# Kernel optimization log

Measured on AMD Instinct MI355X. Metric: run time of the kernel, lower is better.

The kernel has to match this reference:

```python
import jax, jax.numpy as jnp
import numpy as np

B, P, D = 128, 196, 2048      # batch, num_pixels (14*14), encoder_dim
A, E, H, V = 512, 512, 512, 10000  # attention_dim, embedding_size, lstm_size, vocab
T_MAX = 20
T = T_MAX - 1                 # decoder steps = max_length - 1


def setup_inputs() -> dict:
    key = jax.random.key(0)
    ks = jax.random.split(key, 24)
    s = lambda k, sh: (jax.random.normal(k, sh, jnp.float32) * 0.02)
    features = jax.random.normal(ks[0], (B, P, D), jnp.float32)
    captions = jax.random.randint(ks[1], (B, T_MAX), 0, V)
    # sorted-descending ragged lengths in [4, T_MAX]; force max to T_MAX
    lengths = jnp.sort(jax.random.randint(ks[2], (B,), 4, T_MAX + 1))[::-1].at[0].set(T_MAX)
    return dict(
        features=features, captions=captions, lengths=lengths,
        emb=s(ks[3], (V, E)),
        h_fc_w=s(ks[4], (D, H)), h_fc_b=jnp.zeros((H,), jnp.float32),
        c_fc_w=s(ks[5], (D, H)), c_fc_b=jnp.zeros((H,), jnp.float32),
        enc_w=s(ks[6], (D, A)), enc_b=jnp.zeros((A,), jnp.float32),
        dec_w=s(ks[7], (H, A)), dec_b=jnp.zeros((A,), jnp.float32),
        att_w=s(ks[8], (A, 1)), att_b=jnp.zeros((1,), jnp.float32),
        beta_w=s(ks[9], (H, D)), beta_b=jnp.zeros((D,), jnp.float32),
        w_ih=s(ks[10], (D + E, 4 * H)), b_ih=jnp.zeros((4 * H,), jnp.float32),
        w_hh=s(ks[11], (H, 4 * H)), b_hh=jnp.zeros((4 * H,), jnp.float32),
        cls_w=s(ks[12], (H, V)), cls_b=jnp.zeros((V,), jnp.float32),
    )


def reference(features, captions, lengths, emb,
              h_fc_w, h_fc_b, c_fc_w, c_fc_b,
              enc_w, enc_b, dec_w, dec_b, att_w, att_b,
              beta_w, beta_b, w_ih, b_ih, w_hh, b_hh, cls_w, cls_b):
    dec_len = lengths - 1                       # decoder_lengths
    mean_f = features.mean(axis=1)              # [B, D]
    h = mean_f @ h_fc_w + h_fc_b                # [B, H]
    c = mean_f @ c_fc_w + c_fc_b
    att1 = features @ enc_w + enc_b             # [B, P, A] (loop-invariant)
    emb_seq = emb[captions[:, :T]]              # [B, T, E]
    xs = (jnp.moveaxis(emb_seq, 0, 1),          # [T, B, E]
          jnp.arange(T)[:, None] < dec_len[None, :])  # [T, B] step-valid mask

    def step(carry, x):
        h, c = carry
        e_t, m = x                              # [B, E], [B] bool
        att2 = h @ dec_w + dec_b                # [B, A]
        e = jnp.squeeze(jax.nn.relu(att1 + att2[:, None, :]) @ att_w + att_b, -1)  # [B, P]
        alpha = jax.nn.softmax(e, axis=1)
        awe = jnp.einsum('bp,bpd->bd', alpha, features)
        gate = jax.nn.sigmoid(h @ beta_w + beta_b)
        awe = gate * awe
        xin = jnp.concatenate([e_t, awe], axis=1)           # [B, E+D]
        gates = xin @ w_ih + b_ih + h @ w_hh + b_hh         # [B, 4H]
        i, f, g, o = jnp.split(gates, 4, axis=1)
        c_new = jax.nn.sigmoid(f) * c + jax.nn.sigmoid(i) * jnp.tanh(g)
        h_new = jax.nn.sigmoid(o) * jnp.tanh(c_new)
        mf = m[:, None].astype(h.dtype)
        y = (h_new @ cls_w + cls_b) * mf        # rows past their length stay 0
        h = jnp.where(m[:, None], h_new, h)
        c = jnp.where(m[:, None], c_new, c)
        return (h, c), (y, alpha * mf)

    _, (ys, alphas) = jax.lax.scan(step, (h, c), xs)
    y_predicted = jnp.moveaxis(ys, 0, 1)        # [B, T, V]
    alphas = jnp.moveaxis(alphas, 0, 1)         # [B, T, P]
    return y_predicted, alphas
```

## Files before the change

kernel.cpp:

```cpp
#include <hip/hip_runtime.h>
#include <cstdint>
#include <cstddef>


#define DEV __device__ __forceinline__

typedef __attribute__((ext_vector_type(8))) short s16x8;
typedef __attribute__((ext_vector_type(4))) float f32x4;

constexpr int Bb = 128, Pp = 196, Dd = 2048, Aa = 512, Ee = 512, Hh = 512, Vv = 10000;
constexpr int Tt = 19, TMAX = 20;
constexpr int NVP = 10048;

DEV float fbs(short s) {
    union { uint32_t u; float f; } v;
    v.u = ((uint32_t)(uint16_t)s) << 16;
    return v.f;
}
DEV short bfs(float f) {
    union { float f; uint32_t u; } v;
    v.f = f;
    uint32_t u = v.u;
    uint32_t r = (u + 0x7FFFu + ((u >> 16) & 1u)) >> 16;
    return (short)(uint16_t)r;
}
DEV void upk(uint32_t v, float& lo, float& hi) {
    union { uint32_t u; float f; } a, b;
    a.u = v << 16;
    b.u = v & 0xffff0000u;
    lo = a.f;
    hi = b.f;
}

template<int BM, int BN, int BK, int TH, int WR, int WC, int EPI>
__global__ __launch_bounds__(TH) void gemm_k(
    const short* __restrict__ Ag, int lda,
    const short* __restrict__ Bg, int ldb,
    int K,
    float* __restrict__ outF, float* __restrict__ outF2,
    short* __restrict__ outH, short* __restrict__ outH2,
    int ldo,
    const float* __restrict__ bias, const float* __restrict__ bias2,
    const int* __restrict__ lens)
{
    constexpr int NCH = BK / 8;
    constexpr int AU = NCH * BM, BU = NCH * BN;
    constexpr int APT = AU / TH, BPT = BU / TH;
    constexpr int WM = BM / WR, WN = BN / WC;
    constexpr int FM = WM / 16, FN = WN / 16;

    __shared__ __align__(16) short sA[AU * 8];
    __shared__ __align__(16) short sB[BU * 8];

    const int tid = threadIdx.x, lane = tid & 63, wid = tid >> 6;
    const int l15 = lane & 15, l4 = lane >> 4;

    int m0, n0, trow_ = 0;
    if constexpr (EPI == 0) {
        int task = (blockIdx.x & 7) * 49 + (blockIdx.x >> 3);
        m0 = (task >> 1) * BM;
        n0 = (task & 1) * BN;
    } else if constexpr (EPI == 3) {
        const int nwg = (int)gridDim.x;
        const int qq = nwg >> 3, rr = nwg & 7;
        int xcd = (int)blockIdx.x & 7, idx = (int)blockIdx.x >> 3;
        int task = (xcd < rr) ? xcd * (qq + 1) + idx
                              : rr * (qq + 1) + (xcd - rr) * qq + idx;
        int npanel = task / Tt;
        trow_ = task - npanel * Tt;
        m0 = trow_ * BM;
        n0 = npanel * BN;
    } else if constexpr (EPI == 4) {
        m0 = ((int)blockIdx.x & 3) * BM;
        n0 = ((int)blockIdx.x >> 2) * BN;
    } else {
        m0 = blockIdx.y * BM;
        n0 = blockIdx.x * BN;
    }
    const int wr = wid / WC, wc = wid % WC;

    f32x4 acc[FM][FN];
    #pragma unroll
    for (int i = 0; i < FM; ++i)
        #pragma unroll
        for (int j = 0; j < FN; ++j) acc[i][j] = {0.f, 0.f, 0.f, 0.f};

    for (int kt = 0; kt < K; kt += BK) {
        s16x8 ra[APT], rb[BPT];
        #pragma unroll
        for (int i = 0; i < APT; ++i) {
            int q2 = tid + TH * i;
            int r2 = q2 / NCH, ch = q2 % NCH;
            ra[i] = *(const s16x8*)(Ag + (size_t)(m0 + r2) * lda + kt + ch * 8);
        }
        #pragma unroll
        for (int i = 0; i < BPT; ++i) {
            int q2 = tid + TH * i;
            int r2 = q2 / NCH, ch = q2 % NCH;
            rb[i] = *(const s16x8*)(Bg + (size_t)(n0 + r2) * ldb + kt + ch * 8);
        }
        __syncthreads();
        #pragma unroll
        for (int i = 0; i < APT; ++i) {
            int q2 = tid + TH * i;
            int r2 = q2 / NCH, ch = q2 % NCH;
            *(s16x8*)(sA + (r2 * NCH + (ch ^ (r2 & 7))) * 8) = ra[i];
        }
        #pragma unroll
        for (int i = 0; i < BPT; ++i) {
            int q2 = tid + TH * i;
            int r2 = q2 / NCH, ch = q2 % NCH;
            *(s16x8*)(sB + (r2 * NCH + (ch ^ (r2 & 7))) * 8) = rb[i];
        }
        __syncthreads();
        #pragma unroll
        for (int ks = 0; ks < BK / 32; ++ks) {
            s16x8 af[FM], bf[FN];
            #pragma unroll
            for (int fm = 0; fm < FM; ++fm) {
                int rr2 = wr * WM + fm * 16 + l15, cc = ks * 4 + l4;
                af[fm] = *(const s16x8*)&sA[(rr2 * NCH + (cc ^ (rr2 & 7))) * 8];
            }
            #pragma unroll
            for (int fn = 0; fn < FN; ++fn) {
                int rr2 = wc * WN + fn * 16 + l15, cc = ks * 4 + l4;
                bf[fn] = *(const s16x8*)&sB[(rr2 * NCH + (cc ^ (rr2 & 7))) * 8];
            }
            #pragma unroll
            for (int fm = 0; fm < FM; ++fm)
                #pragma unroll
                for (int fn = 0; fn < FN; ++fn)
                    acc[fm][fn] = __builtin_amdgcn_mfma_f32_16x16x32_bf16(af[fm], bf[fn], acc[fm][fn], 0, 0, 0);
        }
        __syncthreads();
    }

    #pragma unroll
    for (int fm = 0; fm < FM; ++fm)
        #pragma unroll
        for (int fn = 0; fn < FN; ++fn)
            #pragma unroll
            for (int r2 = 0; r2 < 4; ++r2) {
                int ml = wr * WM + fm * 16 + l4 * 4 + r2;
                int nl = wc * WN + fn * 16 + l15;
                int m = m0 + ml, n = n0 + nl;
                float v = acc[fm][fn][r2];
                if constexpr (EPI == 0) {
                    outH[(size_t)m * ldo + n] = bfs(v + bias[n]);
                } else if constexpr (EPI == 1) {
                    outH[(size_t)m * ldo + n] = bfs(v);
                } else if constexpr (EPI == 3) {
                    if (n < Vv) {
                        bool mk = trow_ < lens[ml] - 1;
                        outF[((size_t)ml * Tt + trow_) * Vv + n] = mk ? (v + bias[n]) : 0.f;
                    }
                } else if constexpr (EPI == 4) {
                    if (n < 512) outF[(size_t)m * Aa + n] = v + bias[n];
                    else if (n < 2560)
                        outF2[(size_t)m * Dd + (n - 512)] =
                            1.f / (1.f + expf(-(v + bias2[n - 512])));
                    else
                        ((float*)outH)[(size_t)m * 2048 + (n - 2560)] = v;
                } else if constexpr (EPI == 6) {
                    if (n < 512) {
                        outH2[(size_t)m * 512 + n] = bfs(v + bias[n]);
                    } else {
                        outF2[(size_t)m * 512 + (n - 512)] = v + bias2[n - 512];
                    }
                }
            }
}

__global__ __launch_bounds__(512) void att_awe_k(
    const short* __restrict__ att1b, const float* __restrict__ att2b,
    const float* __restrict__ att_w, const float* __restrict__ att_b,
    const short* __restrict__ featb, const float* __restrict__ gatebuf,
    short* __restrict__ xin, float* __restrict__ al_out,
    const int* __restrict__ lens, int t)
{
    const int b = blockIdx.y, half = blockIdx.x;
    const int tid = threadIdx.x, lane = tid & 63, wid = tid >> 6;
    __shared__ float se[224];
    __shared__ float sred[256];
    __shared__ float sal[224];

    float aw[8], a2[8];
    #pragma unroll
    for (int j = 0; j < 8; ++j) {
        aw[j] = att_w[lane * 8 + j];
        a2[j] = att2b[b * 512 + lane * 8 + j];
    }
    float ab = att_b[0];
    for (int p = wid; p < Pp; p += 8) {
        s16x8 row = *(const s16x8*)&att1b[((size_t)b * Pp + p) * 512 + lane * 8];
        float s = 0.f;
        #pragma unroll
        for (int j = 0; j < 8; ++j) {
            float v = fbs(row[j]) + a2[j];
            v = v > 0.f ? v : 0.f;
            s += v * aw[j];
        }
        #pragma unroll
        for (int m = 32; m; m >>= 1) s += __shfl_xor(s, m);
        if (lane == 0) se[p] = s + ab;
    }
    __syncthreads();
    float e = 0.f, ex = 0.f;
    if (tid < 256) {
        e = (tid < Pp) ? se[tid] : -3.0e38f;
        sred[tid] = e;
    }
    __syncthreads();
    for (int st = 128; st > 0; st >>= 1) {
        if (tid < st) sred[tid] = fmaxf(sred[tid], sred[tid + st]);
        __syncthreads();
    }
    float mx = sred[0];
    __syncthreads();
    if (tid < 256) {
        ex = (tid < Pp) ? expf(e - mx) : 0.f;
        sred[tid] = ex;
    }
    __syncthreads();
    for (int st = 128; st > 0; st >>= 1) {
        if (tid < st) sred[tid] += sred[tid + st];
        __syncthreads();
    }
    float inv = 1.f / sred[0];
    if (tid < Pp) {
        float al = ex * inv;
        sal[tid] = al;
        if (half == 0) {
            float mf = (t < lens[b] - 1) ? 1.f : 0.f;
            al_out[((size_t)b * Tt + t) * Pp + tid] = al * mf;
        }
    }
    __syncthreads();
    int d0 = half * 1024 + tid * 2;
    const short* f = featb + (size_t)b * Pp * Dd + d0;
    float s0 = 0.f, s1 = 0.f;
    #pragma unroll 4
    for (int p = 0; p < Pp; ++p) {
        uint32_t v = *(const uint32_t*)(f + (size_t)p * Dd);
        float lo, hi;
        upk(v, lo, hi);
        float al = sal[p];
        s0 += al * lo;
        s1 += al * hi;
    }
    float2 g = *(const float2*)&gatebuf[b * 2048 + d0];
    uint32_t o = ((uint32_t)(uint16_t)bfs(g.y * s1) << 16) | (uint16_t)bfs(g.x * s0);
    *(uint32_t*)(xin + (size_t)b * 2048 + d0) = o;
}

__global__ __launch_bounds__(256) void gates_lstm_k(
    const short* __restrict__ xin, const short* __restrict__ combT,
    const short* __restrict__ eprec, const float* __restrict__ hpart,
    const float* __restrict__ b_ih, const float* __restrict__ b_hh,
    float* __restrict__ c_state, short* __restrict__ hnew_all,
    short* __restrict__ hb16, const int* __restrict__ lens, int t)
{
    constexpr int BM = 32, BN = 32, BK = 128, K = 2048;
    constexpr int NCH = BK / 8;
    constexpr int AU = NCH * BM;
    __shared__ __align__(16) short sA[AU * 8];
    __shared__ __align__(16) short sB[AU * 8];

    const int m0 = ((int)blockIdx.x & 3) * BM, n0 = ((int)blockIdx.x >> 2) * BN;
    const int tid = threadIdx.x, lane = tid & 63, wid = tid >> 6;
    const int l15 = lane & 15, l4 = lane >> 4;
    const int wr = wid >> 1, wc = wid & 1;

    f32x4 acc = {0.f, 0.f, 0.f, 0.f};
    const int r2 = tid / NCH, ch0 = tid % NCH;
    const short* Abase = xin + (size_t)(m0 + r2) * 2048 + ch0 * 8;
    const short* Bbase = combT + (size_t)(n0 + r2) * 2048 + ch0 * 8;
    const size_t rowadv = (size_t)16 * 2048;

    s16x8 raA0, raA1, rbA0, rbA1, raB0, raB1, rbB0, rbB1;

    auto loadA = [&](int kt, s16x8& a0, s16x8& a1, s16x8& b0, s16x8& b1) {
        a0 = *(const s16x8*)(Abase + kt);
        a1 = *(const s16x8*)(Abase + rowadv + kt);
        b0 = *(const s16x8*)(Bbase + kt);
        b1 = *(const s16x8*)(Bbase + rowadv + kt);
    };
    const int sl0 = ((r2) * NCH + (ch0 ^ (r2 & 7))) * 8;
    const int sl1 = ((r2 + 16) * NCH + (ch0 ^ ((r2 + 16) & 7))) * 8;
    auto storeS = [&](s16x8& a0, s16x8& a1, s16x8& b0, s16x8& b1) {
        *(s16x8*)(sA + sl0) = a0;
        *(s16x8*)(sA + sl1) = a1;
        *(s16x8*)(sB + sl0) = b0;
        *(s16x8*)(sB + sl1) = b1;
    };
    const int rrA = wr * 16 + l15, rrB = wc * 16 + l15;
    auto mfmaS = [&]() {
        #pragma unroll
        for (int ks = 0; ks < BK / 32; ++ks) {
            int cc = ks * 4 + l4;
            s16x8 af = *(const s16x8*)&sA[(rrA * NCH + (cc ^ (rrA & 7))) * 8];
            s16x8 bf = *(const s16x8*)&sB[(rrB * NCH + (cc ^ (rrB & 7))) * 8];
            acc = __builtin_amdgcn_mfma_f32_16x16x32_bf16(af, bf, acc, 0, 0, 0);
        }
    };

    loadA(0, raA0, raA1, rbA0, rbA1);
    #pragma unroll 1
    for (int kt = 0; kt < K; kt += 2 * BK) {
        __syncthreads();
        storeS(raA0, raA1, rbA0, rbA1);
        __syncthreads();
        if (kt + BK < K) loadA(kt + BK, raB0, raB1, rbB0, rbB1);
        mfmaS();
        __syncthreads();
        storeS(raB0, raB1, rbB0, rbB1);
        __syncthreads();
        if (kt + 2 * BK < K) loadA(kt + 2 * BK, raA0, raA1, rbA0, rbA1);
        mfmaS();
    }

    __syncthreads();
    float* sE = (float*)sA;
    #pragma unroll
    for (int r = 0; r < 4; ++r) {
        int ml = wr * 16 + l4 * 4 + r, nl = wc * 16 + l15;
        sE[ml * 32 + nl] = acc[r];
    }
    __syncthreads();
    int bl = tid >> 3, jl = tid & 7;
    int b = m0 + bl, q = (n0 >> 2) + jl;
    f32x4 ge = *(const f32x4*)&sE[bl * 32 + jl * 4];
    f32x4 hp = *(const f32x4*)&hpart[(size_t)b * 2048 + n0 + jl * 4];
    short4 ep = *(const short4*)&eprec[((size_t)t * 128 + b) * 2048 + n0 + jl * 4];
    float gi = ge[0] + hp[0] + fbs(ep.x) + b_ih[q]        + b_hh[q];
    float gf = ge[1] + hp[1] + fbs(ep.y) + b_ih[512 + q]  + b_hh[512 + q];
    float gg = ge[2] + hp[2] + fbs(ep.z) + b_ih[1024 + q] + b_hh[1024 + q];
    float go = ge[3] + hp[3] + fbs(ep.w) + b_ih[1536 + q] + b_hh[1536 + q];
    float si = 1.f / (1.f + expf(-gi));
    float sf = 1.f / (1.f + expf(-gf));
    float so = 1.f / (1.f + expf(-go));
    float tg = tanhf(gg);
    int sidx = b * 512 + q;
    float cn = sf * c_state[sidx] + si * tg;
    float hn = so * tanhf(cn);
    hnew_all[((size_t)t * 128 + b) * 512 + q] = bfs(hn);
    if (t < lens[b] - 1) {
        c_state[sidx] = cn;
        hb16[sidx] = bfs(hn);
    }
}

__global__ __launch_bounds__(256) void conv_mean_k(
    const float* __restrict__ feat, short* __restrict__ featb, short* __restrict__ meanb)
{
    int b = blockIdx.y;
    int d = (blockIdx.x * 256 + threadIdx.x) * 2;
    const float* f = feat + (size_t)b * Pp * Dd + d;
    short* o = featb + (size_t)b * Pp * Dd + d;
    float s0 = 0.f, s1 = 0.f;
    #pragma unroll 4
    for (int p = 0; p < Pp; ++p) {
        float2 v = *(const float2*)(f + (size_t)p * Dd);
        s0 += v.x; s1 += v.y;
        uint32_t ov = ((uint32_t)(uint16_t)bfs(v.y) << 16) | (uint16_t)bfs(v.x);
        *(uint32_t*)(o + (size_t)p * Dd) = ov;
    }
    const float inv = 1.f / 196.f;
    uint32_t mv = ((uint32_t)(uint16_t)bfs(s1 * inv) << 16) | (uint16_t)bfs(s0 * inv);
    *(uint32_t*)(meanb + (size_t)b * Dd + d) = mv;
}

DEV void t32(const float* __restrict__ src, int R, int C,
             short* __restrict__ dst, int ds, int off, int perm,
             int local, int gx, float (*tile)[33])
{
    int x = local % gx, y = local / gx;
    int c0 = x * 32, r0 = y * 32;
    int tx = threadIdx.x & 31, ty = threadIdx.x >> 5;
    #pragma unroll
    for (int i = 0; i < 4; ++i) {
        int r = r0 + ty + i * 8, c = c0 + tx;
        tile[ty + i * 8][tx] = (r < R && c < C) ? src[(size_t)r * C + c] : 0.f;
    }
    __syncthreads();
    #pragma unroll
    for (int i = 0; i < 4; ++i) {
        int cc = c0 + ty + i * 8, rr = r0 + tx;
        if (rr < R) {
            int drow = perm ? ((cc & 511) * 4 + (cc >> 9)) : cc;
            dst[(size_t)drow * ds + off + rr] = bfs(tile[tx][ty + i * 8]);
        }
    }
}

__global__ __launch_bounds__(256) void prep_k(
    const float* __restrict__ enc_w, const float* __restrict__ h_fc_w,
    const float* __restrict__ c_fc_w, const float* __restrict__ dec_w,
    const float* __restrict__ beta_w, const float* __restrict__ w_ih,
    const float* __restrict__ w_hh, const float* __restrict__ cls_w,
    const float* __restrict__ emb, const int* __restrict__ caps,
    short* __restrict__ encT, short* __restrict__ hcT, short* __restrict__ catT,
    short* __restrict__ combT, short* __restrict__ wtopT, short* __restrict__ clsT,
    short* __restrict__ embseq)
{
    __shared__ float tile[32][33];
    int bid = blockIdx.x;
    if (bid < 1024)        t32(enc_w, 2048, 512, encT, 2048, 0, 0, bid, 16, tile);
    else if (bid < 2048)   t32(h_fc_w, 2048, 512, hcT, 2048, 0, 0, bid - 1024, 16, tile);
    else if (bid < 3072)   t32(c_fc_w, 2048, 512, hcT + (size_t)512 * 2048, 2048, 0, 0, bid - 2048, 16, tile);
    else if (bid < 3328)   t32(dec_w, 512, 512, catT, 512, 0, 0, bid - 3072, 16, tile);
    else if (bid < 4352)   t32(beta_w, 512, 2048, catT + (size_t)512 * 512, 512, 0, 0, bid - 3328, 64, tile);
    else if (bid < 5376)   t32(w_hh, 512, 2048, catT + (size_t)2560 * 512, 512, 0, 1, bid - 4352, 64, tile);
    else if (bid < 9472)   t32(w_ih + (size_t)512 * 2048, 2048, 2048, combT, 2048, 0, 1, bid - 5376, 64, tile);
    else if (bid < 10496)  t32(w_ih, 512, 2048, wtopT, 512, 0, 1, bid - 9472, 64, tile);
    else if (bid < 15520)  t32(cls_w, 512, 10000, clsT, 512, 0, 0, bid - 10496, 314, tile);
    else {
        size_t i = (size_t)(bid - 15520) * 256 + threadIdx.x;
        if (i < (size_t)Tt * Bb * Ee) {
            int e = (int)(i % Ee);
            size_t r = i / Ee;
            int b = (int)(r % Bb);
            int t = (int)(r / Bb);
            int cap = caps[b * TMAX + t];
            embseq[i] = bfs(emb[(size_t)cap * Ee + e]);
        }
    }
}

extern "C" void kernel_launch(void* const* d_in, const int* in_sizes, int n_in,
                              void* d_out, int out_size, void* d_ws, size_t ws_size,
                              hipStream_t stream)
{
    const float* features = (const float*)d_in[0];
    const int* captions   = (const int*)d_in[1];
    const int* lengths    = (const int*)d_in[2];
    const float* emb      = (const float*)d_in[3];
    const float* h_fc_w   = (const float*)d_in[4];
    const float* h_fc_b   = (const float*)d_in[5];
    const float* c_fc_w   = (const float*)d_in[6];
    const float* c_fc_b   = (const float*)d_in[7];
    const float* enc_w    = (const float*)d_in[8];
    const float* enc_b    = (const float*)d_in[9];
    const float* dec_w    = (const float*)d_in[10];
    const float* dec_b    = (const float*)d_in[11];
    const float* att_w    = (const float*)d_in[12];
    const float* att_b    = (const float*)d_in[13];
    const float* beta_w   = (const float*)d_in[14];
    const float* beta_b   = (const float*)d_in[15];
    const float* w_ih     = (const float*)d_in[16];
    const float* b_ih     = (const float*)d_in[17];
    const float* w_hh     = (const float*)d_in[18];
    const float* b_hh     = (const float*)d_in[19];
    const float* cls_w    = (const float*)d_in[20];
    const float* cls_b    = (const float*)d_in[21];

    char* w = (char*)d_ws;
    auto alloc = [&](size_t bytes) {
        char* p = w;
        w += (bytes + 255) & ~(size_t)255;
        return p;
    };
    short* featb    = (short*)alloc((size_t)Bb * Pp * Dd * 2);
    short* att1b    = (short*)alloc((size_t)Bb * Pp * Aa * 2);
    short* encT     = (short*)alloc((size_t)Aa * Dd * 2);
    short* combT    = (short*)alloc((size_t)2048 * 2048 * 2);
    short* wtopT    = (short*)alloc((size_t)2048 * 512 * 2);
    short* clsT     = (short*)alloc((size_t)NVP * Hh * 2);
    short* catT     = (short*)alloc((size_t)4608 * 512 * 2);
    short* hcT      = (short*)alloc((size_t)1024 * Dd * 2);
    short* embseq   = (short*)alloc((size_t)Tt * Bb * Ee * 2);
    short* meanb    = (short*)alloc((size_t)Bb * Dd * 2);
    short* eprec    = (short*)alloc((size_t)Tt * Bb * 2048 * 2);
    float* c_state  = (float*)alloc((size_t)Bb * Hh * 4);
    float* att2b    = (float*)alloc((size_t)Bb * Aa * 4);
    float* gatebuf  = (float*)alloc((size_t)Bb * Dd * 4);
    float* hpart    = (float*)alloc((size_t)Bb * 2048 * 4);
    short* xin      = (short*)alloc((size_t)Bb * 2048 * 2);
    short* hb16     = (short*)alloc((size_t)Bb * Hh * 2);
    short* hnew_all = (short*)alloc((size_t)Tt * Bb * Hh * 2);

    float* y_out  = (float*)d_out;
    float* al_out = y_out + (size_t)Bb * Tt * Vv;

    conv_mean_k<<<dim3(4, 128), 256, 0, stream>>>(features, featb, meanb);
    prep_k<<<dim3(20384), 256, 0, stream>>>(
        enc_w, h_fc_w, c_fc_w, dec_w, beta_w, w_ih, w_hh, cls_w, emb, captions,
        encT, hcT, catT, combT, wtopT, clsT, embseq);

    gemm_k<128, 64, 64, 256, 2, 2, 6><<<dim3(16, 1), 256, 0, stream>>>(
        meanb, 2048, hcT, 2048, 2048,
        nullptr, c_state, nullptr, hb16, 0, h_fc_b, c_fc_b, nullptr);

    gemm_k<128, 256, 64, 512, 2, 4, 0><<<dim3(392), 512, 0, stream>>>(
        featb, 2048, encT, 2048, 2048,
        nullptr, nullptr, att1b, nullptr, Aa, enc_b, nullptr, nullptr);

    gemm_k<128, 64, 64, 256, 2, 2, 1><<<dim3(32, 19), 256, 0, stream>>>(
        embseq, 512, wtopT, 512, 512,
        nullptr, nullptr, eprec, nullptr, 2048, nullptr, nullptr, nullptr);

    for (int t = 0; t < Tt; ++t) {
        gemm_k<32, 64, 64, 256, 2, 2, 4><<<dim3(288), 256, 0, stream>>>(
            hb16, 512, catT, 512, 512,
            att2b, gatebuf, (short*)hpart, nullptr, 0, dec_b, beta_b, nullptr);
        att_awe_k<<<dim3(2, 128), 512, 0, stream>>>(
            att1b, att2b, att_w, att_b, featb, gatebuf, xin,
            al_out, lengths, t);
        gates_lstm_k<<<dim3(256), 256, 0, stream>>>(
            xin, combT, eprec, hpart, b_ih, b_hh, c_state, hnew_all, hb16,
            lengths, t);
    }

    gemm_k<128, 64, 64, 256, 2, 2, 3><<<dim3(157 * Tt), 256, 0, stream>>>(
        hnew_all, 512, clsT, 512, 512,
        y_out, nullptr, nullptr, nullptr, 0, cls_b, nullptr, lengths);
}
```

Before: 1.356 ms.

## Prefetch GEMM tiles into registers, merge attention halves, widen classifier tiles

The GEMM main loop now issues the global loads for the next K tile into a second register set while MFMAs run on the current shared-memory tile, hiding global latency. The attention/AWE kernel uses one 1024-thread block per batch row instead of two 512-thread blocks, so the energy and softmax phase is no longer computed twice. The classifier GEMM moves to 128-wide N tiles, with vocab padding raised to 10112 and the prep transpose grid adjusted to match. Risks include higher register pressure from the doubled prefetch buffers, and the two-tiles-per-iteration loop assumes K is a multiple of 2*BK.

Result: faster. 1.239 ms (-8.6%).

```diff
diff --git a/kernel.cpp b/kernel.cpp
--- a/kernel.cpp
+++ b/kernel.cpp
@@ -10,7 +10,7 @@
 
 constexpr int Bb = 128, Pp = 196, Dd = 2048, Aa = 512, Ee = 512, Hh = 512, Vv = 10000;
 constexpr int Tt = 19, TMAX = 20;
-constexpr int NVP = 10048;
+constexpr int NVP = 10112;
 
 DEV float fbs(short s) {
     union { uint32_t u; float f; } v;
@@ -85,34 +85,37 @@
         #pragma unroll
         for (int j = 0; j < FN; ++j) acc[i][j] = {0.f, 0.f, 0.f, 0.f};
 
-    for (int kt = 0; kt < K; kt += BK) {
-        s16x8 ra[APT], rb[BPT];
+    s16x8 ra[APT], rb[BPT], ra2[APT], rb2[BPT];
+
+    auto gload = [&](int kt, s16x8 (&pa)[APT], s16x8 (&pb)[BPT]) {
         #pragma unroll
         for (int i = 0; i < APT; ++i) {
             int q2 = tid + TH * i;
             int r2 = q2 / NCH, ch = q2 % NCH;
-            ra[i] = *(const s16x8*)(Ag + (size_t)(m0 + r2) * lda + kt + ch * 8);
+            pa[i] = *(const s16x8*)(Ag + (size_t)(m0 + r2) * lda + kt + ch * 8);
         }
         #pragma unroll
         for (int i = 0; i < BPT; ++i) {
             int q2 = tid + TH * i;
             int r2 = q2 / NCH, ch = q2 % NCH;
-            rb[i] = *(const s16x8*)(Bg + (size_t)(n0 + r2) * ldb + kt + ch * 8);
-        }
-        __syncthreads();
+            pb[i] = *(const s16x8*)(Bg + (size_t)(n0 + r2) * ldb + kt + ch * 8);
+        }
+    };
+    auto sstore = [&](s16x8 (&pa)[APT], s16x8 (&pb)[BPT]) {
         #pragma unroll
         for (int i = 0; i < APT; ++i) {
             int q2 = tid + TH * i;
             int r2 = q2 / NCH, ch = q2 % NCH;
-            *(s16x8*)(sA + (r2 * NCH + (ch ^ (r2 & 7))) * 8) = ra[i];
+            *(s16x8*)(sA + (r2 * NCH + (ch ^ (r2 & 7))) * 8) = pa[i];
         }
         #pragma unroll
         for (int i = 0; i < BPT; ++i) {
             int q2 = tid + TH * i;
             int r2 = q2 / NCH, ch = q2 % NCH;
-            *(s16x8*)(sB + (r2 * NCH + (ch ^ (r2 & 7))) * 8) = rb[i];
-        }
-        __syncthreads();
+            *(s16x8*)(sB + (r2 * NCH + (ch ^ (r2 & 7))) * 8) = pb[i];
+        }
+    };
+    auto domfma = [&]() {
         #pragma unroll
         for (int ks = 0; ks < BK / 32; ++ks) {
             s16x8 af[FM], bf[FN];
@@ -132,7 +135,21 @@
                 for (int fn = 0; fn < FN; ++fn)
                     acc[fm][fn] = __builtin_amdgcn_mfma_f32_16x16x32_bf16(af[fm], bf[fn], acc[fm][fn], 0, 0, 0);
         }
-        __syncthreads();
+    };
+
+    gload(0, ra, rb);
+    #pragma unroll 1
+    for (int kt = 0; kt < K; kt += 2 * BK) {
+        __syncthreads();
+        sstore(ra, rb);
+        __syncthreads();
+        gload(kt + BK, ra2, rb2);
+        domfma();
+        __syncthreads();
+        sstore(ra2, rb2);
+        __syncthreads();
+        if (kt + 2 * BK < K) gload(kt + 2 * BK, ra, rb);
+        domfma();
     }
 
     #pragma unroll
@@ -171,14 +188,14 @@
             }
 }
 
-__global__ __launch_bounds__(512) void att_awe_k(
+__global__ __launch_bounds__(1024) void att_awe_k(
     const short* __restrict__ att1b, const float* __restrict__ att2b,
     const float* __restrict__ att_w, const float* __restrict__ att_b,
     const short* __restrict__ featb, const float* __restrict__ gatebuf,
     short* __restrict__ xin, float* __restrict__ al_out,
     const int* __restrict__ lens, int t)
 {
-    const int b = blockIdx.y, half = blockIdx.x;
+    const int b = blockIdx.x;
     const int tid = threadIdx.x, lane = tid & 63, wid = tid >> 6;
     __shared__ float se[224];
     __shared__ float sred[256];
@@ -191,7 +208,7 @@
         a2[j] = att2b[b * 512 + lane * 8 + j];
     }
     float ab = att_b[0];
-    for (int p = wid; p < Pp; p += 8) {
+    for (int p = wid; p < Pp; p += 16) {
         s16x8 row = *(const s16x8*)&att1b[((size_t)b * Pp + p) * 512 + lane * 8];
         float s = 0.f;
         #pragma unroll
@@ -230,13 +247,11 @@
     if (tid < Pp) {
         float al = ex * inv;
         sal[tid] = al;
-        if (half == 0) {
-            float mf = (t < lens[b] - 1) ? 1.f : 0.f;
-            al_out[((size_t)b * Tt + t) * Pp + tid] = al * mf;
-        }
-    }
-    __syncthreads();
-    int d0 = half * 1024 + tid * 2;
+        float mf = (t < lens[b] - 1) ? 1.f : 0.f;
+        al_out[((size_t)b * Tt + t) * Pp + tid] = al * mf;
+    }
+    __syncthreads();
+    int d0 = tid * 2;
     const short* f = featb + (size_t)b * Pp * Dd + d0;
     float s0 = 0.f, s1 = 0.f;
     #pragma unroll 4
@@ -413,9 +428,9 @@
     else if (bid < 5376)   t32(w_hh, 512, 2048, catT + (size_t)2560 * 512, 512, 0, 1, bid - 4352, 64, tile);
     else if (bid < 9472)   t32(w_ih + (size_t)512 * 2048, 2048, 2048, combT, 2048, 0, 1, bid - 5376, 64, tile);
     else if (bid < 10496)  t32(w_ih, 512, 2048, wtopT, 512, 0, 1, bid - 9472, 64, tile);
-    else if (bid < 15520)  t32(cls_w, 512, 10000, clsT, 512, 0, 0, bid - 10496, 314, tile);
+    else if (bid < 15552)  t32(cls_w, 512, 10000, clsT, 512, 0, 0, bid - 10496, 316, tile);
     else {
-        size_t i = (size_t)(bid - 15520) * 256 + threadIdx.x;
+        size_t i = (size_t)(bid - 15552) * 256 + threadIdx.x;
         if (i < (size_t)Tt * Bb * Ee) {
             int e = (int)(i % Ee);
             size_t r = i / Ee;
@@ -483,7 +498,7 @@
     float* al_out = y_out + (size_t)Bb * Tt * Vv;
 
     conv_mean_k<<<dim3(4, 128), 256, 0, stream>>>(features, featb, meanb);
-    prep_k<<<dim3(20384), 256, 0, stream>>>(
+    prep_k<<<dim3(20416), 256, 0, stream>>>(
         enc_w, h_fc_w, c_fc_w, dec_w, beta_w, w_ih, w_hh, cls_w, emb, captions,
         encT, hcT, catT, combT, wtopT, clsT, embseq);
 
@@ -503,7 +518,7 @@
         gemm_k<32, 64, 64, 256, 2, 2, 4><<<dim3(288), 256, 0, stream>>>(
             hb16, 512, catT, 512, 512,
             att2b, gatebuf, (short*)hpart, nullptr, 0, dec_b, beta_b, nullptr);
-        att_awe_k<<<dim3(2, 128), 512, 0, stream>>>(
+        att_awe_k<<<dim3(128), 1024, 0, stream>>>(
             att1b, att2b, att_w, att_b, featb, gatebuf, xin,
             al_out, lengths, t);
         gates_lstm_k<<<dim3(256), 256, 0, stream>>>(
@@ -511,7 +526,7 @@
             lengths, t);
     }
 
-    gemm_k<128, 64, 64, 256, 2, 2, 3><<<dim3(157 * Tt), 256, 0, stream>>>(
+    gemm_k<128, 128, 64, 256, 2, 2, 3><<<dim3(79 * Tt), 256, 0, stream>>>(
         hnew_all, 512, clsT, 512, 512,
         y_out, nullptr, nullptr, nullptr, 0, cls_b, nullptr, lengths);
 }
```
